# Performance work log

Hardware: AMD Instinct MI355X
Metric: run time of the kernel (lower is better)

The kernel has to match this reference:

```python
import jax, jax.numpy as jnp
import numpy as np


def _gcn_conv(x, src, dst, num_nodes, W, b):
    """PyG GCNConv: add self-loops, symmetric normalization, scatter-add, bias."""
    h = x @ W  # [N, F_out]
    # degree over destination nodes (all edge weights are 1, incl. self-loops)
    deg = jax.ops.segment_sum(jnp.ones_like(dst, dtype=h.dtype), dst,
                              num_segments=num_nodes)
    deg_inv_sqrt = jnp.where(deg > 0, jax.lax.rsqrt(deg), 0.0)
    norm = deg_inv_sqrt[src] * deg_inv_sqrt[dst]  # [E+N]
    msg = h[src] * norm[:, None]                  # gather + scale
    out = jax.ops.segment_sum(msg, dst, num_segments=num_nodes)  # scatter-add
    return out + b


def setup_inputs() -> dict:
    key = jax.random.key(0)
    k_x, k_e, k_w1, k_w2 = jax.random.split(key, 4)
    N, E, F = 50000, 800000, 128
    x = jax.random.normal(k_x, (N, F), dtype=jnp.float32)
    edge_index = jax.random.randint(k_e, (2, E), 0, N, dtype=jnp.int64)
    scale = 1.0 / np.sqrt(F)
    W1 = jax.random.normal(k_w1, (F, F), dtype=jnp.float32) * scale
    b1 = jnp.zeros((F,), dtype=jnp.float32)
    W2 = jax.random.normal(k_w2, (F, F), dtype=jnp.float32) * scale
    b2 = jnp.zeros((F,), dtype=jnp.float32)
    return {"x": x, "edge_index": edge_index, "W1": W1, "b1": b1,
            "W2": W2, "b2": b2}


def reference(x, edge_index, W1, b1, W2, b2):
    num_nodes = x.shape[0]
    loops = jnp.arange(num_nodes, dtype=edge_index.dtype)
    src = jnp.concatenate([edge_index[0], loops])
    dst = jnp.concatenate([edge_index[1], loops])
    # layer 1: GCNConv -> Identity norm -> relu -> dropout(eval=identity)
    h = jax.nn.relu(_gcn_conv(x, src, dst, num_nodes, W1, b1))
    # layer 2 (last_activation=True, so relu again)
    out = jax.nn.relu(_gcn_conv(h, src, dst, num_nodes, W2, b2))
    return out
```

## Files before the change

kernel.cpp:

```cpp
#include <hip/hip_runtime.h>
#include <hip/hip_bf16.h>

#define CDIV(a,b) (((a)+(b)-1)/(b))

typedef __bf16 bf16x8 __attribute__((ext_vector_type(8)));
typedef float  f32x4  __attribute__((ext_vector_type(4)));

union Frag16 { uint4 u; bf16x8 f; unsigned short s[8]; };
union Pack8  { unsigned short s[4]; uint2 u; };

__device__ __forceinline__ unsigned short f2bf(float f) {
    unsigned u = __float_as_uint(f);
    return (unsigned short)((u + 0x7fff + ((u >> 16) & 1)) >> 16);
}
__device__ __forceinline__ float bf2f(unsigned short s) {
    return __uint_as_float(((unsigned)s) << 16);
}

__device__ __forceinline__ int load_src(const int* e, int f, int E, int i) {
    return f ? e[i] : e[2 * i];
}
__device__ __forceinline__ int load_dst(const int* e, int f, int E, int i) {
    return f ? e[E + i] : e[2 * (E + i)];
}

__global__ __launch_bounds__(256) void prep_kernel(const float* __restrict__ W1,
                                                   const float* __restrict__ W2,
                                                   unsigned short* __restrict__ Wf1h,
                                                   unsigned short* __restrict__ Wf1l,
                                                   unsigned short* __restrict__ Wf2h,
                                                   unsigned short* __restrict__ Wf2l,
                                                   const int* __restrict__ edges,
                                                   int* __restrict__ flag, int E,
                                                   int4* __restrict__ zero_base, int Z4) {
    int tid = threadIdx.x;
    if (blockIdx.x == 2) {
        if (tid == 0) *flag = 0;
        __syncthreads();
        int n = min(E, 4096);
        int found = 0;
        for (int j = tid; j < n; j += 256) found |= (edges[2 * j + 1] != 0);
        if (found) *flag = 1;
        return;
    }
    if (blockIdx.x >= 3) {
        int idx = (blockIdx.x - 3) * 256 + tid;
        if (idx < Z4) zero_base[idx] = make_int4(0, 0, 0, 0);
        return;
    }
    const float* W = (blockIdx.x == 0) ? W1 : W2;
    unsigned short* Wfh = (blockIdx.x == 0) ? Wf1h : Wf2h;
    unsigned short* Wfl = (blockIdx.x == 0) ? Wf1l : Wf2l;
    #pragma unroll
    for (int it = 0; it < 8; ++it) {
        int c = it * 256 + tid;
        int ntk = c >> 6;
        int lane = c & 63;
        int ks = ntk & 3;
        int ntile = ntk >> 2;
        int quad = lane >> 4, nlo = lane & 15;
        int n = ntile * 16 + nlo;
        Frag16 h, l;
        #pragma unroll
        for (int j = 0; j < 8; ++j) {
            float w = W[(ks * 32 + quad * 8 + j) * 128 + n];
            h.s[j] = f2bf(w);
            float rr = w - bf2f(h.s[j]);
            l.s[j] = f2bf(rr);
        }
        *(uint4*)(Wfh + (size_t)c * 8) = h.u;
        *(uint4*)(Wfl + (size_t)c * 8) = l.u;
    }
}

__device__ __forceinline__ void gemm_body(const float* __restrict__ X,
                                          const unsigned short* __restrict__ Wfh,
                                          const unsigned short* __restrict__ Wfl,
                                          unsigned short* __restrict__ out16,
                                          int N, int blk,
                                          unsigned short (*Xh)[136],
                                          unsigned short (*Xl)[136]) {
    int tid = threadIdx.x;
    int row0 = blk * 64;
    #pragma unroll
    for (int it = 0; it < 8; ++it) {
        int f = it * 256 + tid;
        int r = f >> 5, c4 = f & 31;
        float4 v = make_float4(0.f, 0.f, 0.f, 0.f);
        int gr = row0 + r;
        if (gr < N) v = *(const float4*)(X + (size_t)gr * 128 + c4 * 4);
        float vv[4] = {v.x, v.y, v.z, v.w};
        Pack8 h, l;
        #pragma unroll
        for (int j = 0; j < 4; ++j) {
            h.s[j] = f2bf(vv[j]);
            float rr = vv[j] - bf2f(h.s[j]);
            l.s[j] = f2bf(rr);
        }
        *(uint2*)(&Xh[r][c4 * 4]) = h.u;
        *(uint2*)(&Xl[r][c4 * 4]) = l.u;
    }
    __syncthreads();

    int lane = tid & 63;
    int wv = tid >> 6;
    int quad = lane >> 4, nlo = lane & 15;
    f32x4 acc[8];
    #pragma unroll
    for (int t = 0; t < 8; ++t) acc[t] = (f32x4){0.f, 0.f, 0.f, 0.f};

    #pragma unroll
    for (int ks = 0; ks < 4; ++ks) {
        int kcol = ks * 32 + quad * 8;
        Frag16 xh, xl;
        xh.u = *(const uint4*)(&Xh[wv * 16 + nlo][kcol]);
        xl.u = *(const uint4*)(&Xl[wv * 16 + nlo][kcol]);
        #pragma unroll
        for (int t = 0; t < 8; ++t) {
            size_t cidx = ((size_t)(t * 4 + ks) * 64 + lane) * 8;
            Frag16 wh, wl;
            wh.u = *(const uint4*)(Wfh + cidx);
            wl.u = *(const uint4*)(Wfl + cidx);
            acc[t] = __builtin_amdgcn_mfma_f32_16x16x32_bf16(xh.f, wh.f, acc[t], 0, 0, 0);
            acc[t] = __builtin_amdgcn_mfma_f32_16x16x32_bf16(xh.f, wl.f, acc[t], 0, 0, 0);
            acc[t] = __builtin_amdgcn_mfma_f32_16x16x32_bf16(xl.f, wh.f, acc[t], 0, 0, 0);
        }
    }
    #pragma unroll
    for (int rg = 0; rg < 4; ++rg) {
        int gr = row0 + wv * 16 + quad * 4 + rg;
        if (gr < N) {
            #pragma unroll
            for (int t = 0; t < 8; ++t)
                out16[(size_t)gr * 128 + t * 16 + nlo] = f2bf(acc[t][rg]);
        }
    }
}

__global__ __launch_bounds__(256) void fat_kernel(const float* __restrict__ X,
                                                  const unsigned short* __restrict__ Wfh,
                                                  const unsigned short* __restrict__ Wfl,
                                                  unsigned short* __restrict__ out16,
                                                  int N, int Ggemm,
                                                  const int* __restrict__ edges,
                                                  const int* __restrict__ flag,
                                                  int* __restrict__ counts_sh,
                                                  int* __restrict__ rank, int E) {
    __shared__ unsigned short Xh[64][136];
    __shared__ unsigned short Xl[64][136];
    if (blockIdx.x < (unsigned)Ggemm) {
        gemm_body(X, Wfh, Wfl, out16, N, blockIdx.x, Xh, Xl);
        return;
    }
    int e = (blockIdx.x - Ggemm) * 256 + threadIdx.x;
    if (e >= E) return;
    int f = *flag;
    int d = load_dst(edges, f, E, e);
    int s = blockIdx.x & 7;
    int r = atomicAdd(&counts_sh[s * N + d], 1);
    rank[e] = (r << 3) | s;
}

#define BSUM_FLAG 0x40000000
__global__ __launch_bounds__(256) void merge_scan_kernel(int* __restrict__ counts_sh,
                                                         float* __restrict__ dis,
                                                         int* __restrict__ bsum,
                                                         int* __restrict__ row_ptr,
                                                         int N, int E) {
    __shared__ int red[4];
    __shared__ int wsum[4];
    __shared__ int boff_sh;
    int tid = threadIdx.x;
    int bid = blockIdx.x;
    if (bid == 0 && tid == 0) row_ptr[N] = E;
    int base = bid * 1024 + tid * 4;
    int cnt[4];
    int bs = 0;
    #pragma unroll
    for (int j = 0; j < 4; ++j) {
        int d = base + j;
        cnt[j] = 0;
        if (d < N) {
            int run = 0;
            #pragma unroll
            for (int s = 0; s < 8; ++s) {
                int v = counts_sh[s * N + d];
                counts_sh[s * N + d] = run;
                run += v;
            }
            cnt[j] = run;
            dis[d] = rsqrtf((float)(run + 1));
            bs += run;
        }
    }
    int t = bs;
    #pragma unroll
    for (int off = 32; off >= 1; off >>= 1) t += __shfl_down(t, off, 64);
    if ((tid & 63) == 0) red[tid >> 6] = t;
    __syncthreads();
    if (tid == 0) {
        int total = red[0] + red[1] + red[2] + red[3];
        __hip_atomic_store(&bsum[bid], total | BSUM_FLAG,
                           __ATOMIC_RELEASE, __HIP_MEMORY_SCOPE_AGENT);
    }
    if (tid < 64) {
        int sum = 0;
        for (int p = tid; p < bid; p += 64) {
            int v;
            do {
                v = __hip_atomic_load(&bsum[p], __ATOMIC_ACQUIRE,
                                      __HIP_MEMORY_SCOPE_AGENT);
                if (!(v & BSUM_FLAG)) __builtin_amdgcn_s_sleep(1);
            } while (!(v & BSUM_FLAG));
            sum += v & (BSUM_FLAG - 1);
        }
        #pragma unroll
        for (int off = 32; off >= 1; off >>= 1) sum += __shfl_down(sum, off, 64);
        if (tid == 0) boff_sh = sum;
    }
    __syncthreads();
    int lane = tid & 63, wv = tid >> 6;
    int tsum = cnt[0] + cnt[1] + cnt[2] + cnt[3];
    int x = tsum;
    #pragma unroll
    for (int off = 1; off < 64; off <<= 1) {
        int u = __shfl_up(x, off, 64);
        if (lane >= off) x += u;
    }
    int texcl = x - tsum;
    if (lane == 63) wsum[wv] = x;
    __syncthreads();
    int woff = 0;
    for (int w = 0; w < wv; ++w) woff += wsum[w];
    int off0 = boff_sh + woff + texcl;
    int run = 0;
    #pragma unroll
    for (int j = 0; j < 4; ++j) {
        if (base + j < N) row_ptr[base + j] = off0 + run;
        run += cnt[j];
    }
}

__global__ void fill_kernel(const int* __restrict__ edges, const int* __restrict__ flag,
                            const int* __restrict__ row_ptr, const int* __restrict__ rank,
                            const int* __restrict__ counts_sh,
                            const float* __restrict__ dis, int2* __restrict__ edata,
                            int E, int N) {
    int e = blockIdx.x * blockDim.x + threadIdx.x;
    if (e >= E) return;
    int f = *flag;
    int s = load_src(edges, f, E, e);
    int d = load_dst(edges, f, E, e);
    int rk = rank[e];
    int sh = rk & 7;
    int pos = row_ptr[d] + counts_sh[sh * N + d] + (rk >> 3);
    edata[pos] = make_int2(s, __float_as_int(dis[s]));
}

__global__ __launch_bounds__(1024) void agg1_fused_kernel(
        const unsigned short* __restrict__ A16,
        const int* __restrict__ row_ptr,
        const int2* __restrict__ edata,
        const float* __restrict__ dis,
        const float* __restrict__ bias,
        const unsigned short* __restrict__ Wfh,
        const unsigned short* __restrict__ Wfl,
        unsigned short* __restrict__ H1out, int N) {
    __shared__ unsigned short Hl[16][128];
    int wv = threadIdx.x >> 6;
    int lane = threadIdx.x & 63;
    int wid = blockIdx.x * 16 + wv;
    if (wid < N) {
        const ushort2* H2 = (const ushort2*)A16;
        float dd = dis[wid];
        ushort2 hv = H2[(size_t)wid * 64 + lane];
        float wself = dd * dd;
        float2 acc = make_float2(bf2f(hv.x) * wself, bf2f(hv.y) * wself);
        int e0 = __builtin_amdgcn_readfirstlane(row_ptr[wid]);
        int e1 = __builtin_amdgcn_readfirstlane(row_ptr[wid + 1]);
        for (int e = e0; e < e1; e += 8) {
            int rem = e1 - e;
            int   sj[8];
            float wj[8];
            #pragma unroll
            for (int j = 0; j < 8; ++j) {
                bool valid = j < rem;
                int2 ed = edata[valid ? e + j : e];
                sj[j] = ed.x;
                wj[j] = valid ? __int_as_float(ed.y) * dd : 0.f;
            }
            ushort2 aj[8];
            #pragma unroll
            for (int j = 0; j < 8; ++j)
                aj[j] = H2[(size_t)sj[j] * 64 + lane];
            #pragma unroll
            for (int j = 0; j < 8; ++j) {
                acc.x += bf2f(aj[j].x) * wj[j];
                acc.y += bf2f(aj[j].y) * wj[j];
            }
        }
        float2 b = ((const float2*)bias)[lane];
        float ox = fmaxf(acc.x + b.x, 0.f);
        float oy = fmaxf(acc.y + b.y, 0.f);
        int c = (lane * 2) ^ ((wv & 7) << 3);
        *(ushort2*)(&Hl[wv][c]) = make_ushort2(f2bf(ox), f2bf(oy));
    }
    __syncthreads();
    if (wv >= 8) return;
    int quad = lane >> 4, nlo = lane & 15;
    f32x4 acc = (f32x4){0.f, 0.f, 0.f, 0.f};
    #pragma unroll
    for (int ks = 0; ks < 4; ++ks) {
        int cb = (ks * 32 + quad * 8) ^ ((nlo & 7) << 3);
        Frag16 xa, wh, wl;
        xa.u = *(const uint4*)(&Hl[nlo][cb]);
        size_t cidx = ((size_t)(wv * 4 + ks) * 64 + lane) * 8;
        wh.u = *(const uint4*)(Wfh + cidx);
        wl.u = *(const uint4*)(Wfl + cidx);
        acc = __builtin_amdgcn_mfma_f32_16x16x32_bf16(xa.f, wh.f, acc, 0, 0, 0);
        acc = __builtin_amdgcn_mfma_f32_16x16x32_bf16(xa.f, wl.f, acc, 0, 0, 0);
    }
    #pragma unroll
    for (int rg = 0; rg < 4; ++rg) {
        int gr = blockIdx.x * 16 + quad * 4 + rg;
        if (gr < N)
            H1out[(size_t)gr * 128 + wv * 16 + nlo] = f2bf(acc[rg]);
    }
}

__global__ __launch_bounds__(256) void agg2_kernel(const unsigned short* __restrict__ H16,
                                                   const int* __restrict__ row_ptr,
                                                   const int2* __restrict__ edata,
                                                   const float* __restrict__ dis,
                                                   const float* __restrict__ bias,
                                                   float* __restrict__ outp, int N) {
    int wid = (blockIdx.x * blockDim.x + threadIdx.x) >> 6;
    int lane = threadIdx.x & 63;
    if (wid >= N) return;
    const ushort2* H2 = (const ushort2*)H16;
    float dd = dis[wid];
    ushort2 hv = H2[(size_t)wid * 64 + lane];
    float wself = dd * dd;
    float2 acc = make_float2(bf2f(hv.x) * wself, bf2f(hv.y) * wself);
    int e0 = __builtin_amdgcn_readfirstlane(row_ptr[wid]);
    int e1 = __builtin_amdgcn_readfirstlane(row_ptr[wid + 1]);
    for (int e = e0; e < e1; e += 16) {
        int rem = e1 - e;
        int   sj[16];
        float wj[16];
        #pragma unroll
        for (int j = 0; j < 16; ++j) {
            bool valid = j < rem;
            int2 ed = edata[valid ? e + j : e];
            sj[j] = ed.x;
            wj[j] = valid ? __int_as_float(ed.y) * dd : 0.f;
        }
        ushort2 aj[16];
        #pragma unroll
        for (int j = 0; j < 16; ++j)
            aj[j] = H2[(size_t)sj[j] * 64 + lane];
        #pragma unroll
        for (int j = 0; j < 16; ++j) {
            acc.x += bf2f(aj[j].x) * wj[j];
            acc.y += bf2f(aj[j].y) * wj[j];
        }
    }
    float2 b = ((const float2*)bias)[lane];
    float ox = fmaxf(acc.x + b.x, 0.f);
    float oy = fmaxf(acc.y + b.y, 0.f);
    ((float2*)outp)[(size_t)wid * 64 + lane] = make_float2(ox, oy);
}

extern "C" void kernel_launch(void* const* d_in, const int* in_sizes, int n_in,
                              void* d_out, int out_size, void* d_ws, size_t ws_size,
                              hipStream_t stream) {
    const float* x    = (const float*)d_in[0];
    const int*  edges = (const int*)d_in[1];
    const float* W1   = (const float*)d_in[2];
    const float* b1   = (const float*)d_in[3];
    const float* W2   = (const float*)d_in[4];
    const float* b2   = (const float*)d_in[5];
    float* out = (float*)d_out;

    const int F = 128;
    const int N = in_sizes[0] / F;
    const int E = in_sizes[1] / 2;
    const int NB = CDIV(N, 1024);
    const int Ggemm = CDIV(N, 64);
    const int Gcount = CDIV(E, 256);

    #define AL4(v) (((v) + 3) & ~3)
    unsigned short* A16 = (unsigned short*)d_ws;
    unsigned short* H1  = A16 + (size_t)AL4(N * F);
    float* dis      = (float*)(H1 + (size_t)AL4(N * F));
    int*  counts_sh = (int*)(dis + AL4(N));
    int*  bsum      = counts_sh + AL4(8 * N);
    int*  flag      = bsum + 64;
    int*  row_ptr   = flag + 4;
    int*  rank      = row_ptr + AL4(N + 1);
    int2* edata     = (int2*)(rank + AL4(E));
    unsigned short* Wf1h = (unsigned short*)(edata + E);
    unsigned short* Wf1l = Wf1h + 16384;
    unsigned short* Wf2h = Wf1l + 16384;
    unsigned short* Wf2l = Wf2h + 16384;

    const int Z4 = (AL4(8 * N) + 64) / 4;
    const int Gprep = 3 + CDIV(Z4, 256);

    prep_kernel<<<Gprep, 256, 0, stream>>>(W1, W2, Wf1h, Wf1l, Wf2h, Wf2l,
                                           edges, flag, E, (int4*)counts_sh, Z4);
    fat_kernel<<<Ggemm + Gcount, 256, 0, stream>>>(x, Wf1h, Wf1l, A16, N, Ggemm,
                                                   edges, flag, counts_sh, rank, E);
    merge_scan_kernel<<<NB, 256, 0, stream>>>(counts_sh, dis, bsum, row_ptr, N, E);
    fill_kernel<<<Gcount, 256, 0, stream>>>(edges, flag, row_ptr, rank,
                                            counts_sh, dis, edata, E, N);

    agg1_fused_kernel<<<CDIV(N, 16), 1024, 0, stream>>>(A16, row_ptr, edata, dis,
                                                        b1, Wf2h, Wf2l, H1, N);
    agg2_kernel<<<CDIV(N * 64, 256), 256, 0, stream>>>(H1, row_ptr, edata, dis, b2, out, N);
}
```

Baseline: 215.3 us.

## Gather neighbor rows with 16-byte loads split across four edge groups per wave

The two aggregation kernels now have each wave split into four 16-lane groups. Each group reads a full 256-byte bf16 feature row with uint4 loads and handles every fourth edge, and the groups' partial sums are combined with cross-lane shuffles. Previously all 64 lanes read 4 bytes each from one edge at a time. The aim is to issue fewer, wider memory instructions per gathered row and to have more independent edges in flight. In exchange each lane keeps eight accumulators, the shuffle reduction adds instructions, and after the reduction only a quarter of the lanes do the epilogue. The LDS swizzle for the fused GEMM is adjusted to match the new 16-byte writes.

```diff
diff --git a/kernel.cpp b/kernel.cpp
--- a/kernel.cpp
+++ b/kernel.cpp
@@ -257,6 +257,43 @@
     edata[pos] = make_int2(s, __float_as_int(dis[s]));
 }
 
+__device__ __forceinline__ void gather_wide(const uint4* __restrict__ H4,
+                                            const int2* __restrict__ edata,
+                                            int e0, int e1, int g, int fl,
+                                            float dd, float wself,
+                                            float acc[8], int wid) {
+    Frag16 u;
+    u.u = H4[(size_t)wid * 16 + fl];
+    #pragma unroll
+    for (int j = 0; j < 8; ++j) acc[j] = bf2f(u.s[j]) * wself;
+    for (int e = e0; e < e1; e += 16) {
+        int2 ed[4]; float w[4];
+        #pragma unroll
+        for (int it = 0; it < 4; ++it) {
+            int idx = e + it * 4 + g;
+            bool valid = idx < e1;
+            ed[it] = edata[valid ? idx : e0];
+            w[it] = valid ? __int_as_float(ed[it].y) * dd : 0.f;
+        }
+        uint4 rv[4];
+        #pragma unroll
+        for (int it = 0; it < 4; ++it)
+            rv[it] = H4[(size_t)ed[it].x * 16 + fl];
+        #pragma unroll
+        for (int it = 0; it < 4; ++it) {
+            Frag16 r; r.u = rv[it];
+            #pragma unroll
+            for (int j = 0; j < 8; ++j)
+                acc[j] += bf2f(r.s[j]) * w[it];
+        }
+    }
+    #pragma unroll
+    for (int j = 0; j < 8; ++j) {
+        acc[j] += __shfl_xor(acc[j], 16, 64);
+        acc[j] += __shfl_xor(acc[j], 32, 64);
+    }
+}
+
 __global__ __launch_bounds__(1024) void agg1_fused_kernel(
         const unsigned short* __restrict__ A16,
         const int* __restrict__ row_ptr,
@@ -270,61 +307,46 @@
     int wv = threadIdx.x >> 6;
     int lane = threadIdx.x & 63;
     int wid = blockIdx.x * 16 + wv;
+    int g = lane >> 4, fl = lane & 15;
     if (wid < N) {
-        const ushort2* H2 = (const ushort2*)A16;
-        float dd = dis[wid];
-        ushort2 hv = H2[(size_t)wid * 64 + lane];
-        float wself = dd * dd;
-        float2 acc = make_float2(bf2f(hv.x) * wself, bf2f(hv.y) * wself);
+        float dd = __uint_as_float(
+            __builtin_amdgcn_readfirstlane(__float_as_uint(dis[wid])));
         int e0 = __builtin_amdgcn_readfirstlane(row_ptr[wid]);
         int e1 = __builtin_amdgcn_readfirstlane(row_ptr[wid + 1]);
-        for (int e = e0; e < e1; e += 8) {
-            int rem = e1 - e;
-            int   sj[8];
-            float wj[8];
-            #pragma unroll
-            for (int j = 0; j < 8; ++j) {
-                bool valid = j < rem;
-                int2 ed = edata[valid ? e + j : e];
-                sj[j] = ed.x;
-                wj[j] = valid ? __int_as_float(ed.y) * dd : 0.f;
-            }
-            ushort2 aj[8];
+        float acc[8];
+        gather_wide((const uint4*)A16, edata, e0, e1, g, fl, dd,
+                    (g == 0) ? dd * dd : 0.f, acc, wid);
+        if (g == 0) {
+            float4 b0 = ((const float4*)bias)[fl * 2];
+            float4 b1 = ((const float4*)bias)[fl * 2 + 1];
+            float bb[8] = {b0.x, b0.y, b0.z, b0.w, b1.x, b1.y, b1.z, b1.w};
+            Frag16 p;
             #pragma unroll
             for (int j = 0; j < 8; ++j)
-                aj[j] = H2[(size_t)sj[j] * 64 + lane];
-            #pragma unroll
-            for (int j = 0; j < 8; ++j) {
-                acc.x += bf2f(aj[j].x) * wj[j];
-                acc.y += bf2f(aj[j].y) * wj[j];
-            }
-        }
-        float2 b = ((const float2*)bias)[lane];
-        float ox = fmaxf(acc.x + b.x, 0.f);
-        float oy = fmaxf(acc.y + b.y, 0.f);
-        int c = (lane * 2) ^ ((wv & 7) << 3);
-        *(ushort2*)(&Hl[wv][c]) = make_ushort2(f2bf(ox), f2bf(oy));
+                p.s[j] = f2bf(fmaxf(acc[j] + bb[j], 0.f));
+            *(uint4*)((char*)&Hl[wv][0] + ((fl * 16) ^ ((wv & 7) << 4))) = p.u;
+        }
     }
     __syncthreads();
     if (wv >= 8) return;
     int quad = lane >> 4, nlo = lane & 15;
-    f32x4 acc = (f32x4){0.f, 0.f, 0.f, 0.f};
+    f32x4 acc2 = (f32x4){0.f, 0.f, 0.f, 0.f};
     #pragma unroll
     for (int ks = 0; ks < 4; ++ks) {
-        int cb = (ks * 32 + quad * 8) ^ ((nlo & 7) << 3);
+        int cb = (64 * ks + 16 * quad) ^ ((nlo & 7) << 4);
         Frag16 xa, wh, wl;
-        xa.u = *(const uint4*)(&Hl[nlo][cb]);
+        xa.u = *(const uint4*)((const char*)&Hl[nlo][0] + cb);
         size_t cidx = ((size_t)(wv * 4 + ks) * 64 + lane) * 8;
         wh.u = *(const uint4*)(Wfh + cidx);
         wl.u = *(const uint4*)(Wfl + cidx);
-        acc = __builtin_amdgcn_mfma_f32_16x16x32_bf16(xa.f, wh.f, acc, 0, 0, 0);
-        acc = __builtin_amdgcn_mfma_f32_16x16x32_bf16(xa.f, wl.f, acc, 0, 0, 0);
+        acc2 = __builtin_amdgcn_mfma_f32_16x16x32_bf16(xa.f, wh.f, acc2, 0, 0, 0);
+        acc2 = __builtin_amdgcn_mfma_f32_16x16x32_bf16(xa.f, wl.f, acc2, 0, 0, 0);
     }
     #pragma unroll
     for (int rg = 0; rg < 4; ++rg) {
         int gr = blockIdx.x * 16 + quad * 4 + rg;
         if (gr < N)
-            H1out[(size_t)gr * 128 + wv * 16 + nlo] = f2bf(acc[rg]);
+            H1out[(size_t)gr * 128 + wv * 16 + nlo] = f2bf(acc2[rg]);
     }
 }
 
@@ -337,38 +359,29 @@
     int wid = (blockIdx.x * blockDim.x + threadIdx.x) >> 6;
     int lane = threadIdx.x & 63;
     if (wid >= N) return;
-    const ushort2* H2 = (const ushort2*)H16;
-    float dd = dis[wid];
-    ushort2 hv = H2[(size_t)wid * 64 + lane];
-    float wself = dd * dd;
-    float2 acc = make_float2(bf2f(hv.x) * wself, bf2f(hv.y) * wself);
+    int g = lane >> 4, fl = lane & 15;
+    float dd = __uint_as_float(
+        __builtin_amdgcn_readfirstlane(__float_as_uint(dis[wid])));
     int e0 = __builtin_amdgcn_readfirstlane(row_ptr[wid]);
     int e1 = __builtin_amdgcn_readfirstlane(row_ptr[wid + 1]);
-    for (int e = e0; e < e1; e += 16) {
-        int rem = e1 - e;
-        int   sj[16];
-        float wj[16];
-        #pragma unroll
-        for (int j = 0; j < 16; ++j) {
-            bool valid = j < rem;
-            int2 ed = edata[valid ? e + j : e];
-            sj[j] = ed.x;
-            wj[j] = valid ? __int_as_float(ed.y) * dd : 0.f;
-        }
-        ushort2 aj[16];
-        #pragma unroll
-        for (int j = 0; j < 16; ++j)
-            aj[j] = H2[(size_t)sj[j] * 64 + lane];
-        #pragma unroll
-        for (int j = 0; j < 16; ++j) {
-            acc.x += bf2f(aj[j].x) * wj[j];
-            acc.y += bf2f(aj[j].y) * wj[j];
-        }
-    }
-    float2 b = ((const float2*)bias)[lane];
-    float ox = fmaxf(acc.x + b.x, 0.f);
-    float oy = fmaxf(acc.y + b.y, 0.f);
-    ((float2*)outp)[(size_t)wid * 64 + lane] = make_float2(ox, oy);
+    float acc[8];
+    gather_wide((const uint4*)H16, edata, e0, e1, g, fl, dd,
+                (g == 0) ? dd * dd : 0.f, acc, wid);
+    if (g != 0) return;
+    float4 b0 = ((const float4*)bias)[fl * 2];
+    float4 b1 = ((const float4*)bias)[fl * 2 + 1];
+    float bb[8] = {b0.x, b0.y, b0.z, b0.w, b1.x, b1.y, b1.z, b1.w};
+    float4 o0, o1;
+    o0.x = fmaxf(acc[0] + bb[0], 0.f);
+    o0.y = fmaxf(acc[1] + bb[1], 0.f);
+    o0.z = fmaxf(acc[2] + bb[2], 0.f);
+    o0.w = fmaxf(acc[3] + bb[3], 0.f);
+    o1.x = fmaxf(acc[4] + bb[4], 0.f);
+    o1.y = fmaxf(acc[5] + bb[5], 0.f);
+    o1.z = fmaxf(acc[6] + bb[6], 0.f);
+    o1.w = fmaxf(acc[7] + bb[7], 0.f);
+    ((float4*)outp)[(size_t)wid * 32 + fl * 2]     = o0;
+    ((float4*)outp)[(size_t)wid * 32 + fl * 2 + 1] = o1;
 }
 
 extern "C" void kernel_launch(void* const* d_in, const int* in_sizes, int n_in,
```

New measurement: 227.6 us. 5.7% more time.
